# Kernel optimization log

Measured on AMD Instinct MI355X. Metric: run time of the kernel, lower is better.

The kernel has to match this reference:

```python
import jax, jax.numpy as jnp
import numpy as np

N_GRAM = 3

def setup_inputs() -> dict:
    key = jax.random.key(0)
    k1, k2, k3, k4, k5, k6 = jax.random.split(key, 6)
    B, L, D = 4, 2048, 1024
    hidden_states = jax.random.normal(k1, (B, L, D), dtype=jnp.float32)
    input_ids = jax.random.randint(k2, (B, L), 0, 32, dtype=jnp.int64)
    s = 1.0 / np.sqrt(D)
    W1 = jax.random.normal(k3, (D, D), dtype=jnp.float32) * s
    b1 = jax.random.normal(k4, (D,), dtype=jnp.float32) * s
    W2 = jax.random.normal(k5, (D, D), dtype=jnp.float32) * s
    b2 = jax.random.normal(k6, (D,), dtype=jnp.float32) * s
    return {"hidden_states": hidden_states, "input_ids": input_ids,
            "W1": W1, "b1": b1, "W2": W2, "b2": b2}

def _ngram_mask(input_ids, n, seq_len):
    # ngrams[b, i, :] = input_ids[b, i:i+n]  -> [B, L-n+1, n]
    L = input_ids.shape[1]
    ngrams = jnp.stack([input_ids[:, j:L - n + 1 + j] for j in range(n)], axis=-1)
    # left-pad n-1 zero rows along seq dim -> [B, L, n]
    padded = jnp.pad(ngrams, ((0, 0), (n - 1, 0), (0, 0)))
    # pairwise ngram equality -> [B, L, L]
    mask = jnp.all(padded[:, :, None, :] == padded[:, None, :, :], axis=-1)
    # strictly-causal (diagonal=-1)
    causal = jnp.tril(jnp.ones((seq_len, seq_len), dtype=bool), k=-1)
    return mask & causal[None, :, :]

def reference(hidden_states, input_ids, W1, b1, W2, b2):
    B, L, D = hidden_states.shape
    mask = _ngram_mask(input_ids, N_GRAM, L)  # [B, L, L] bool
    num_attended = jnp.maximum(mask.sum(axis=-1, keepdims=True), 1)  # [B, L, 1]
    weights = mask.astype(hidden_states.dtype) / num_attended.astype(hidden_states.dtype)
    pooled = jnp.einsum('bij,bjd->bid', weights, hidden_states)
    direct_path = hidden_states @ W1 + b1
    ngram_path = pooled @ W2 + b2
    return direct_path + ngram_path
```

## Files before the change

### kernel.cpp

```cpp
#include <hip/hip_runtime.h>
#include <hip/hip_bf16.h>
#include <stdint.h>

#define LSEQ 2048
#define DDIM 1024

typedef __attribute__((ext_vector_type(8))) short bf16x8;
typedef __attribute__((ext_vector_type(16))) float f32x16;

__device__ __forceinline__ ushort f2bf(float x) {
    uint32_t u = __builtin_bit_cast(uint32_t, x);
    u += 0x7fffu + ((u >> 16) & 1u);
    return (ushort)(u >> 16);
}

__device__ __forceinline__ void stage16(const void* g, void* lds) {
    __builtin_amdgcn_global_load_lds((const __attribute__((address_space(1))) void*)g,
                                     (__attribute__((address_space(3))) void*)lds, 16, 0, 0);
}

__device__ __forceinline__ int swz_off(int row, int k) {
    return row * 2048 + ((k >> 6) << 7) + ((((k >> 3) & 7) ^ (row & 7)) << 4) + ((k & 7) << 1);
}

__device__ __forceinline__ size_t frag_off(int blk, int k16, int lane) {
    return ((size_t)(blk * 64 + k16) * 64 + lane) * 16;
}

__global__ __launch_bounds__(256) void prep(const float* __restrict__ H,
                                            const int* __restrict__ ids,
                                            const float* __restrict__ W1,
                                            const float* __restrict__ W2,
                                            char* __restrict__ Hb,
                                            char* __restrict__ W1t,
                                            char* __restrict__ W2F,
                                            char* __restrict__ PactF,
                                            int* __restrict__ lrow,
                                            int* __restrict__ pcnt) {
    const int bid = blockIdx.x;
    const int tid = threadIdx.x;
    if (bid < 512) {
        __shared__ __align__(16) int sk[LSEQ];
        __shared__ __align__(16) int kk[LSEQ];
        __shared__ unsigned long long wmask[4];
        __shared__ int larow[32];
        __shared__ unsigned bm[8];
        const int grp = bid >> 4, g = bid & 15;
        const int b = grp >> 3, chunk = grp & 7;
        const int base = b * LSEQ;
        const int lane = tid & 63, wid = tid >> 6;

        for (int c = tid; c < LSEQ; c += 256) sk[c] = ids[base + c];
        __syncthreads();
        for (int c = tid; c < LSEQ; c += 256)
            kk[c] = c >= 2 ? ((sk[c - 2] << 10) | (sk[c - 1] << 5) | sk[c]) : 0;
        __syncthreads();

        const int i = chunk * 256 + tid;
        const int ki = kk[i];
        int cnt = 0;
        const int4* k4 = (const int4*)kk;
        const int nq = i >> 2;
        for (int q = 0; q < nq; ++q) {
            int4 v = k4[q];
            cnt += (v.x == ki) + (v.y == ki) + (v.z == ki) + (v.w == ki);
        }
        for (int j2 = nq << 2; j2 < i; ++j2) cnt += (kk[j2] == ki);

        unsigned long long m = __ballot(cnt > 0);
        if (lane == 0) wmask[wid] = m;
        __syncthreads();
        int rank = (int)__popcll(m & ((1ull << lane) - 1ull));
        #pragma unroll
        for (int w = 0; w < 4; ++w) if (w < wid) rank += (int)__popcll(wmask[w]);
        const int na0 = (int)(__popcll(wmask[0]) + __popcll(wmask[1]) +
                              __popcll(wmask[2]) + __popcll(wmask[3]));
        const int na = na0 > 32 ? 32 : na0;
        if (cnt > 0 && rank < 32) larow[rank] = tid;
        if (g == 0 && cnt > 0 && rank < 32) lrow[grp * 32 + rank] = tid;
        if (g == 0 && tid == 0) pcnt[grp] = na;
        __syncthreads();

        const float4* H4 = (const float4*)H;
        for (int e = g; e < na; e += 16) {
            const int i2 = chunk * 256 + larow[e];
            const int ki2 = kk[i2];
            float4 acc = make_float4(0.f, 0.f, 0.f, 0.f);
            int count = 0;
            for (int j0 = 0; j0 < i2; j0 += 256) {
                if (tid < 8) bm[tid] = 0u;
                __syncthreads();
                int j = j0 + tid;
                if (j < i2 && kk[j] == ki2)
                    atomicOr(&bm[tid >> 5], 1u << (tid & 31));
                __syncthreads();
                #pragma unroll
                for (int w = 0; w < 8; ++w) {
                    unsigned mm2 = bm[w];
                    while (mm2) {
                        int bit = __ffs(mm2) - 1;
                        mm2 &= mm2 - 1;
                        int j2 = j0 + w * 32 + bit;
                        count++;
                        float4 h = H4[(size_t)(base + j2) * (DDIM / 4) + tid];
                        acc.x += h.x; acc.y += h.y; acc.z += h.z; acc.w += h.w;
                    }
                }
                __syncthreads();
            }
            float s2 = 1.0f / (float)(count > 0 ? count : 1);
            ushort4 o;
            o.x = f2bf(acc.x * s2); o.y = f2bf(acc.y * s2);
            o.z = f2bf(acc.z * s2); o.w = f2bf(acc.w * s2);
            const int c4 = tid * 4;
            const int flane = e + ((c4 >> 3) & 1) * 32;
            *(ushort4*)(PactF + frag_off(grp, c4 >> 4, flane) + (c4 & 7) * 2) = o;
        }
    } else if (bid < 768) {
        int r2 = bid - 512;
        int k0 = (r2 & 15) * 64, n0 = (r2 >> 4) * 64;
        __shared__ ushort t[64][65];
        #pragma unroll
        for (int it = 0; it < 16; ++it) {
            int idx = it * 256 + tid;
            int r = idx >> 6, c = idx & 63;
            t[c][r] = f2bf(W1[(size_t)(k0 + r) * DDIM + n0 + c]);
        }
        __syncthreads();
        #pragma unroll
        for (int it = 0; it < 4; ++it) {
            int idx = it * 256 + tid;
            int r = idx >> 4, gg = idx & 15;
            ushort4 v;
            v.x = t[r][gg * 4]; v.y = t[r][gg * 4 + 1];
            v.z = t[r][gg * 4 + 2]; v.w = t[r][gg * 4 + 3];
            *(ushort4*)(W1t + swz_off(n0 + r, k0 + gg * 4)) = v;
        }
    } else if (bid < 1024) {
        int r2 = bid - 768;
        int k0 = (r2 & 15) * 64, n0 = (r2 >> 4) * 64;
        __shared__ ushort t[64][65];
        #pragma unroll
        for (int it = 0; it < 16; ++it) {
            int idx = it * 256 + tid;
            int r = idx >> 6, c = idx & 63;
            t[c][r] = f2bf(W2[(size_t)(k0 + r) * DDIM + n0 + c]);
        }
        __syncthreads();
        #pragma unroll
        for (int it = 0; it < 4; ++it) {
            int idx = it * 256 + tid;
            int r = idx >> 4, gg = idx & 15;
            int n = n0 + r, k = k0 + gg * 4;
            ushort4 v;
            v.x = t[r][gg * 4]; v.y = t[r][gg * 4 + 1];
            v.z = t[r][gg * 4 + 2]; v.w = t[r][gg * 4 + 3];
            int flane = (n & 31) + ((k >> 3) & 1) * 32;
            *(ushort4*)(W2F + frag_off(n >> 5, k >> 4, flane) + (k & 7) * 2) = v;
        }
    } else {
        int r0 = (bid - 1024) * 8;
        #pragma unroll
        for (int rr = 0; rr < 8; ++rr) {
            int row = r0 + rr;
            float4 h = *(const float4*)(H + (size_t)row * DDIM + tid * 4);
            ushort4 o;
            o.x = f2bf(h.x); o.y = f2bf(h.y); o.z = f2bf(h.z); o.w = f2bf(h.w);
            *(ushort4*)(Hb + swz_off(row, tid * 4)) = o;
        }
    }
}

__global__ __launch_bounds__(512, 2) void gemm_main(
    const char* __restrict__ Hb,
    const char* __restrict__ W1t,
    const char* __restrict__ PactF,
    const char* __restrict__ W2F,
    const float* __restrict__ b1,
    const float* __restrict__ b2,
    const int* __restrict__ lrow,
    const int* __restrict__ pcnt,
    float* __restrict__ out)
{
    __shared__ __align__(128) char smem[147456];

    const int tid = threadIdx.x;
    const int lane = tid & 63;
    const int wid = tid >> 6;
    const int wr = wid >> 1, wc = wid & 1;
    const int l31 = lane & 31;
    const int hi2 = lane >> 5;
    const int x7 = l31 & 7;

    const int bid = blockIdx.x;
    const int j = bid >> 3;
    const int row0 = ((bid & 7) * 4 + (j >> 3)) * 256;
    const int col0 = (j & 7) * 128;
    const int grp = row0 >> 8;
    const int colblk = col0 >> 5;

    f32x16 acc[2][2];
    #pragma unroll
    for (int mm = 0; mm < 2; ++mm)
        #pragma unroll
        for (int nn = 0; nn < 2; ++nn)
            #pragma unroll
            for (int q = 0; q < 16; ++q) acc[mm][nn][q] = 0.f;
    f32x16 mini;
    #pragma unroll
    for (int q = 0; q < 16; ++q) mini[q] = 0.f;

    const int o_lin = wid * 1024 + lane * 16;
    const int srow = o_lin >> 7;
    const int sbyte = o_lin & 127;

    char* Acur = smem;           char* Anx1 = smem + 32768;  char* Anx2 = smem + 65536;
    char* Bcur = smem + 98304;   char* Bnx1 = smem + 114688; char* Bnx2 = smem + 131072;

    auto stageB = [&](char* dstB, int kb) {
        #pragma unroll
        for (int c = 0; c < 2; ++c)
            stage16(W1t + (size_t)(col0 + c * 64 + srow) * 2048 + kb + sbyte,
                    dstB + c * 8192 + wid * 1024);
    };
    auto stageA = [&](char* dstA, int kb) {
        #pragma unroll
        for (int c = 0; c < 4; ++c)
            stage16(Hb + (size_t)(row0 + c * 64 + srow) * 2048 + kb + sbyte,
                    dstA + c * 8192 + wid * 1024);
    };
    auto computeFat = [&]() {
        bf16x8 af[2][4], bf[2][4];
        #pragma unroll
        for (int ks = 0; ks < 4; ++ks) {
            const int so = ((ks * 2 + hi2) ^ x7) << 4;
            #pragma unroll
            for (int mm = 0; mm < 2; ++mm)
                af[mm][ks] = *(const bf16x8*)(Acur + (wr * 64 + mm * 32 + l31) * 128 + so);
            #pragma unroll
            for (int nn = 0; nn < 2; ++nn)
                bf[nn][ks] = *(const bf16x8*)(Bcur + (wc * 64 + nn * 32 + l31) * 128 + so);
        }
        __builtin_amdgcn_s_setprio(1);
        #pragma unroll
        for (int ks = 0; ks < 4; ++ks)
            #pragma unroll
            for (int mm = 0; mm < 2; ++mm)
                #pragma unroll
                for (int nn = 0; nn < 2; ++nn)
                    acc[mm][nn] = __builtin_amdgcn_mfma_f32_32x32x16_bf16(
                        af[mm][ks], bf[nn][ks], acc[mm][nn], 0, 0, 0);
        __builtin_amdgcn_s_setprio(0);
    };
    auto rotate = [&]() {
        char* tp;
        tp = Acur; Acur = Anx1; Anx1 = Anx2; Anx2 = tp;
        tp = Bcur; Bcur = Bnx1; Bnx1 = Bnx2; Bnx2 = tp;
    };

    stageA(Acur, 0);        stageB(Bcur, 0);
    stageA(Anx1, 1 << 7);   stageB(Bnx1, 1 << 7);
    asm volatile("s_waitcnt vmcnt(6)" ::: "memory");
    __builtin_amdgcn_s_barrier();

    #pragma unroll 1
    for (int t = 0; t < 16; ++t) {
        bf16x8 pa0, pa1, pa2, pa3, wb0, wb1, wb2, wb3;
        if (wid < 4) {
            const int k16 = t * 4;
            pa0 = *(const bf16x8*)(PactF + frag_off(grp, k16 + 0, lane));
            pa1 = *(const bf16x8*)(PactF + frag_off(grp, k16 + 1, lane));
            pa2 = *(const bf16x8*)(PactF + frag_off(grp, k16 + 2, lane));
            pa3 = *(const bf16x8*)(PactF + frag_off(grp, k16 + 3, lane));
            wb0 = *(const bf16x8*)(W2F + frag_off(colblk + wid, k16 + 0, lane));
            wb1 = *(const bf16x8*)(W2F + frag_off(colblk + wid, k16 + 1, lane));
            wb2 = *(const bf16x8*)(W2F + frag_off(colblk + wid, k16 + 2, lane));
            wb3 = *(const bf16x8*)(W2F + frag_off(colblk + wid, k16 + 3, lane));
        }
        if (t < 14) {
            stageA(Anx2, (t + 2) << 7);
            stageB(Bnx2, (t + 2) << 7);
        }
        computeFat();
        if (wid < 4) {
            mini = __builtin_amdgcn_mfma_f32_32x32x16_bf16(pa0, wb0, mini, 0, 0, 0);
            mini = __builtin_amdgcn_mfma_f32_32x32x16_bf16(pa1, wb1, mini, 0, 0, 0);
            mini = __builtin_amdgcn_mfma_f32_32x32x16_bf16(pa2, wb2, mini, 0, 0, 0);
            mini = __builtin_amdgcn_mfma_f32_32x32x16_bf16(pa3, wb3, mini, 0, 0, 0);
        }
        asm volatile("s_waitcnt vmcnt(6)" ::: "memory");
        __builtin_amdgcn_s_barrier();
        rotate();
    }

    asm volatile("s_waitcnt vmcnt(0)" ::: "memory");
    __syncthreads();
    float* miniLDS = (float*)smem;
    int* inv = (int*)(smem + 16384);
    const int na = pcnt[grp];
    if (tid < 256) inv[tid] = -1;
    __syncthreads();
    if (tid < na) inv[lrow[grp * 32 + tid]] = tid;
    if (wid < 4) {
        #pragma unroll
        for (int reg = 0; reg < 16; ++reg) {
            int s = (reg & 3) + 8 * (reg >> 2) + 4 * hi2;
            miniLDS[s * 128 + wid * 32 + l31] = mini[reg];
        }
    }
    __syncthreads();

    #pragma unroll
    for (int mm = 0; mm < 2; ++mm) {
        #pragma unroll
        for (int nn = 0; nn < 2; ++nn) {
            const int cl = wc * 64 + nn * 32 + l31;
            const int c = col0 + cl;
            const float bias = b1[c] + b2[c];
            const int rbase = wr * 64 + mm * 32 + hi2 * 4;
            #pragma unroll
            for (int reg = 0; reg < 16; ++reg) {
                int rl = rbase + (reg & 3) + 8 * (reg >> 2);
                int s = inv[rl];
                float v = acc[mm][nn][reg] + bias;
                if (s >= 0) v += miniLDS[s * 128 + cl];
                out[(size_t)(row0 + rl) * DDIM + c] = v;
            }
        }
    }
}

extern "C" void kernel_launch(void* const* d_in, const int* in_sizes, int n_in,
                              void* d_out, int out_size, void* d_ws, size_t ws_size,
                              hipStream_t stream) {
    const float* H  = (const float*)d_in[0];
    const int*   ids = (const int*)d_in[1];
    const float* W1 = (const float*)d_in[2];
    const float* b1 = (const float*)d_in[3];
    const float* W2 = (const float*)d_in[4];
    const float* b2 = (const float*)d_in[5];
    float* out = (float*)d_out;

    char* ws = (char*)d_ws;
    char* Hb     = ws;
    char* W1t    = ws + (16 << 20);
    char* W2F    = ws + (18 << 20);
    char* PactF  = ws + (20 << 20);
    int* lrow    = (int*)(ws + (22 << 20));
    int* pcnt    = (int*)(ws + (22 << 20) + (8 << 10));

    prep<<<2048, 256, 0, stream>>>(H, ids, W1, W2, Hb, W1t, W2F, PactF, lrow, pcnt);
    gemm_main<<<256, 512, 0, stream>>>(Hb, W1t, PactF, W2F, b1, b2, lrow, pcnt, out);
}
```

Baseline: 67.83 us.

## Shrink GEMM tile to 128x128 with 256 threads and single-buffered LDS

The main GEMM drops from 256x128 tiles with 512 threads and a triple-buffered LDS pipeline to 128x128 tiles with 256 threads and a single 32KB LDS buffer. The grid doubles to 512 blocks, and every wave now does the small ngram-path MFMA. The inverse row map is offset by the block's half-group row. The goal is more resident blocks per CU and a lower LDS footprint. The cost is losing the prefetch overlap: each iteration waits on vmcnt(0) before computing, and each block loads W1 columns with less reuse.

```diff
diff --git a/kernel.cpp b/kernel.cpp
--- a/kernel.cpp
+++ b/kernel.cpp
@@ -171,7 +171,7 @@
     }
 }
 
-__global__ __launch_bounds__(512, 2) void gemm_main(
+__global__ __launch_bounds__(256, 3) void gemm_main(
     const char* __restrict__ Hb,
     const char* __restrict__ W1t,
     const char* __restrict__ PactF,
@@ -182,7 +182,7 @@
     const int* __restrict__ pcnt,
     float* __restrict__ out)
 {
-    __shared__ __align__(128) char smem[147456];
+    __shared__ __align__(128) char smem[32768];
 
     const int tid = threadIdx.x;
     const int lane = tid & 63;
@@ -194,9 +194,10 @@
 
     const int bid = blockIdx.x;
     const int j = bid >> 3;
-    const int row0 = ((bid & 7) * 4 + (j >> 3)) * 256;
+    const int row0 = ((bid & 7) * 8 + (j >> 3)) * 128;
     const int col0 = (j & 7) * 128;
     const int grp = row0 >> 8;
+    const int h0 = row0 & 255;
     const int colblk = col0 >> 5;
 
     f32x16 acc[2][2];
@@ -210,63 +211,25 @@
     #pragma unroll
     for (int q = 0; q < 16; ++q) mini[q] = 0.f;
 
+    char* As = smem;
+    char* Bs = smem + 16384;
     const int o_lin = wid * 1024 + lane * 16;
     const int srow = o_lin >> 7;
     const int sbyte = o_lin & 127;
 
-    char* Acur = smem;           char* Anx1 = smem + 32768;  char* Anx2 = smem + 65536;
-    char* Bcur = smem + 98304;   char* Bnx1 = smem + 114688; char* Bnx2 = smem + 131072;
-
-    auto stageB = [&](char* dstB, int kb) {
-        #pragma unroll
-        for (int c = 0; c < 2; ++c)
-            stage16(W1t + (size_t)(col0 + c * 64 + srow) * 2048 + kb + sbyte,
-                    dstB + c * 8192 + wid * 1024);
-    };
-    auto stageA = [&](char* dstA, int kb) {
-        #pragma unroll
-        for (int c = 0; c < 4; ++c)
-            stage16(Hb + (size_t)(row0 + c * 64 + srow) * 2048 + kb + sbyte,
-                    dstA + c * 8192 + wid * 1024);
-    };
-    auto computeFat = [&]() {
-        bf16x8 af[2][4], bf[2][4];
-        #pragma unroll
-        for (int ks = 0; ks < 4; ++ks) {
-            const int so = ((ks * 2 + hi2) ^ x7) << 4;
-            #pragma unroll
-            for (int mm = 0; mm < 2; ++mm)
-                af[mm][ks] = *(const bf16x8*)(Acur + (wr * 64 + mm * 32 + l31) * 128 + so);
-            #pragma unroll
-            for (int nn = 0; nn < 2; ++nn)
-                bf[nn][ks] = *(const bf16x8*)(Bcur + (wc * 64 + nn * 32 + l31) * 128 + so);
-        }
-        __builtin_amdgcn_s_setprio(1);
-        #pragma unroll
-        for (int ks = 0; ks < 4; ++ks)
-            #pragma unroll
-            for (int mm = 0; mm < 2; ++mm)
-                #pragma unroll
-                for (int nn = 0; nn < 2; ++nn)
-                    acc[mm][nn] = __builtin_amdgcn_mfma_f32_32x32x16_bf16(
-                        af[mm][ks], bf[nn][ks], acc[mm][nn], 0, 0, 0);
-        __builtin_amdgcn_s_setprio(0);
-    };
-    auto rotate = [&]() {
-        char* tp;
-        tp = Acur; Acur = Anx1; Anx1 = Anx2; Anx2 = tp;
-        tp = Bcur; Bcur = Bnx1; Bnx1 = Bnx2; Bnx2 = tp;
-    };
-
-    stageA(Acur, 0);        stageB(Bcur, 0);
-    stageA(Anx1, 1 << 7);   stageB(Bnx1, 1 << 7);
-    asm volatile("s_waitcnt vmcnt(6)" ::: "memory");
-    __builtin_amdgcn_s_barrier();
-
     #pragma unroll 1
     for (int t = 0; t < 16; ++t) {
+        const int kb = t << 7;
+        #pragma unroll
+        for (int c = 0; c < 4; ++c)
+            stage16(Hb + (size_t)(row0 + c * 32 + srow) * 2048 + kb + sbyte,
+                    As + c * 4096 + wid * 1024);
+        #pragma unroll
+        for (int c = 0; c < 4; ++c)
+            stage16(W1t + (size_t)(col0 + c * 32 + srow) * 2048 + kb + sbyte,
+                    Bs + c * 4096 + wid * 1024);
         bf16x8 pa0, pa1, pa2, pa3, wb0, wb1, wb2, wb3;
-        if (wid < 4) {
+        {
             const int k16 = t * 4;
             pa0 = *(const bf16x8*)(PactF + frag_off(grp, k16 + 0, lane));
             pa1 = *(const bf16x8*)(PactF + frag_off(grp, k16 + 1, lane));
@@ -277,35 +240,52 @@
             wb2 = *(const bf16x8*)(W2F + frag_off(colblk + wid, k16 + 2, lane));
             wb3 = *(const bf16x8*)(W2F + frag_off(colblk + wid, k16 + 3, lane));
         }
-        if (t < 14) {
-            stageA(Anx2, (t + 2) << 7);
-            stageB(Bnx2, (t + 2) << 7);
-        }
-        computeFat();
-        if (wid < 4) {
-            mini = __builtin_amdgcn_mfma_f32_32x32x16_bf16(pa0, wb0, mini, 0, 0, 0);
-            mini = __builtin_amdgcn_mfma_f32_32x32x16_bf16(pa1, wb1, mini, 0, 0, 0);
-            mini = __builtin_amdgcn_mfma_f32_32x32x16_bf16(pa2, wb2, mini, 0, 0, 0);
-            mini = __builtin_amdgcn_mfma_f32_32x32x16_bf16(pa3, wb3, mini, 0, 0, 0);
-        }
-        asm volatile("s_waitcnt vmcnt(6)" ::: "memory");
+        asm volatile("s_waitcnt vmcnt(0)" ::: "memory");
         __builtin_amdgcn_s_barrier();
-        rotate();
-    }
-
-    asm volatile("s_waitcnt vmcnt(0)" ::: "memory");
+
+        bf16x8 af[2][4], bf[2][4];
+        #pragma unroll
+        for (int ks = 0; ks < 4; ++ks) {
+            const int so = ((ks * 2 + hi2) ^ x7) << 4;
+            #pragma unroll
+            for (int mm = 0; mm < 2; ++mm)
+                af[mm][ks] = *(const bf16x8*)(As + (wr * 64 + mm * 32 + l31) * 128 + so);
+            #pragma unroll
+            for (int nn = 0; nn < 2; ++nn)
+                bf[nn][ks] = *(const bf16x8*)(Bs + (wc * 64 + nn * 32 + l31) * 128 + so);
+        }
+        __builtin_amdgcn_s_setprio(1);
+        #pragma unroll
+        for (int ks = 0; ks < 4; ++ks)
+            #pragma unroll
+            for (int mm = 0; mm < 2; ++mm)
+                #pragma unroll
+                for (int nn = 0; nn < 2; ++nn)
+                    acc[mm][nn] = __builtin_amdgcn_mfma_f32_32x32x16_bf16(
+                        af[mm][ks], bf[nn][ks], acc[mm][nn], 0, 0, 0);
+        __builtin_amdgcn_s_setprio(0);
+        mini = __builtin_amdgcn_mfma_f32_32x32x16_bf16(pa0, wb0, mini, 0, 0, 0);
+        mini = __builtin_amdgcn_mfma_f32_32x32x16_bf16(pa1, wb1, mini, 0, 0, 0);
+        mini = __builtin_amdgcn_mfma_f32_32x32x16_bf16(pa2, wb2, mini, 0, 0, 0);
+        mini = __builtin_amdgcn_mfma_f32_32x32x16_bf16(pa3, wb3, mini, 0, 0, 0);
+        __builtin_amdgcn_s_barrier();
+    }
+
     __syncthreads();
     float* miniLDS = (float*)smem;
     int* inv = (int*)(smem + 16384);
-    const int na = pcnt[grp];
-    if (tid < 256) inv[tid] = -1;
+    if (tid < 128) inv[tid] = -1;
+    #pragma unroll
+    for (int reg = 0; reg < 16; ++reg) {
+        int s = (reg & 3) + 8 * (reg >> 2) + 4 * hi2;
+        miniLDS[s * 128 + wid * 32 + l31] = mini[reg];
+    }
     __syncthreads();
-    if (tid < na) inv[lrow[grp * 32 + tid]] = tid;
-    if (wid < 4) {
-        #pragma unroll
-        for (int reg = 0; reg < 16; ++reg) {
-            int s = (reg & 3) + 8 * (reg >> 2) + 4 * hi2;
-            miniLDS[s * 128 + wid * 32 + l31] = mini[reg];
+    {
+        const int na = pcnt[grp];
+        if (tid < na) {
+            int rel = lrow[grp * 32 + tid] - h0;
+            if (rel >= 0 && rel < 128) inv[rel] = tid;
         }
     }
     __syncthreads();
@@ -350,5 +330,5 @@
     int* pcnt    = (int*)(ws + (22 << 20) + (8 << 10));
 
     prep<<<2048, 256, 0, stream>>>(H, ids, W1, W2, Hb, W1t, W2F, PactF, lrow, pcnt);
-    gemm_main<<<256, 512, 0, stream>>>(Hb, W1t, PactF, W2F, b1, b2, lrow, pcnt, out);
-}
+    gemm_main<<<512, 256, 0, stream>>>(Hb, W1t, PactF, W2F, b1, b2, lrow, pcnt, out);
+}
```

After: 127.8 us. 88.4% more time.
